# Kernel tuning notes

Measured on AMD Instinct MI355X. Metric: run time of the kernel, lower is better.

## Reference

```python
import jax, jax.numpy as jnp
import numpy as np

# Module hyper-parameters (from init_kwargs)
NDIM = 2
KSIZE = [3, 3]            # must be odd per ConvSP checks
DILATION = [0.05, 0.05]
RADIUS = 0.1
C_IN, C_OUT = 64, 64
B, N = 2, 2048


def _offsets():
    # Kernel-cell center offsets relative to the particle, row-major over dims
    # (matches the cartesian ordering of the original C extension).
    axes = [(np.arange(k) - (k - 1) / 2.0) * d for k, d in zip(KSIZE, DILATION)]
    grids = np.meshgrid(*axes, indexing='ij')
    return np.stack([g.reshape(-1) for g in grids], axis=-1).astype(np.float32)  # [ncells, D]


def setup_inputs() -> dict:
    key = jax.random.key(0)
    k1, k2, k3, k4, k5, k6 = jax.random.split(key, 6)
    pos = jax.random.uniform(k1, (B, N, NDIM), dtype=jnp.float32)          # coords in [0,1]^D
    invmass = jax.random.uniform(k2, (B, N), dtype=jnp.float32) * 0.9 + 0.1  # avoid 1/0
    locs = jnp.concatenate([pos, invmass[..., None]], axis=-1)             # [B,N,D+1]
    data = jax.random.normal(k3, (B, C_IN, N), dtype=jnp.float32)
    density = jax.random.uniform(k4, (B, N), dtype=jnp.float32) + 0.5      # strictly positive
    ncells = int(np.prod(KSIZE))
    weight = jax.random.normal(k5, (C_OUT, C_IN, ncells), dtype=jnp.float32) * 0.05
    bias = jax.random.normal(k6, (C_OUT,), dtype=jnp.float32) * 0.05
    return {"locs": locs, "data": data, "density": density, "weight": weight, "bias": bias}


def _convsp(locs, data, density, weight, bias):
    # SPH interpolation at each kernel-cell query point r_{i,k} = x_i + off_k:
    #   field[b,c,i,k] = sum_j (m_j / rho_j) * data[b,c,j] * W(|x_j - r_{i,k}|, RADIUS)
    # with m_j = 1/invmass_j, then a 1x1-style contraction with weight over (c,k).
    pos = locs[..., :NDIM]                               # [B,N,D]
    invmass = locs[..., NDIM]                            # [B,N]
    coef = 1.0 / (invmass * density)                     # m_j / rho_j, [B,N]
    dcoef = data * coef[:, None, :]                      # [B,C,N]
    diff = pos[:, :, None, :] - pos[:, None, :, :]       # x_i - x_j, [B,N,N,D]
    r2 = RADIUS * RADIUS
    knorm = 315.0 / (64.0 * np.pi * RADIUS ** 9)         # poly6 smoothing kernel norm
    offs = _offsets()                                    # [ncells, D]
    bsz, n = pos.shape[0], pos.shape[1]
    out = jnp.broadcast_to(bias[None, :, None], (bsz, weight.shape[0], n))
    for k in range(offs.shape[0]):                       # fixed small ncells=9 loop
        # |x_j - x_i - off| == |(x_i - x_j) + off|
        d2 = jnp.sum((diff + offs[k]) ** 2, axis=-1)     # [B,N,N] (i = query, j = neighbor)
        w = jnp.where(d2 < r2, (r2 - d2) ** 3, 0.0) * knorm
        field = jnp.einsum('bcj,bij->bci', dcoef, w)     # gather-weighted average
        out = out + jnp.einsum('oc,bci->boi', weight[:, :, k], field)
    return out


def reference(locs, data, density, weight, bias):
    return _convsp(locs, data, density, weight, bias)
```

## Files before the change

### kernel.cpp

```cpp
#include <hip/hip_runtime.h>
#include <hip/hip_bf16.h>
#include <stdint.h>

#define BATCH 2
#define NPTS  2048
#define CIN   64
#define COUT  64
#define NCELL 9

#define KNORM 1.5666851e9f
#define R2 0.01f

typedef __attribute__((ext_vector_type(8))) __bf16 bf16x8;
typedef __attribute__((ext_vector_type(4))) float  f32x4;

union B8 { uint4 u; bf16x8 v; };

static __device__ __forceinline__ unsigned pk2(float a, float b) {
    union { __hip_bfloat162 h; unsigned u; } cv;
    cv.h = __float22bfloat162_rn(make_float2(a, b));
    return cv.u;
}


__global__ __launch_bounds__(256) void prep_kernel(
    const float* __restrict__ locs, const float* __restrict__ data,
    const float* __restrict__ density, const float* __restrict__ weight,
    const float* __restrict__ bias,
    float2* __restrict__ posT, uint16_t* __restrict__ dC,
    uint16_t* __restrict__ WB, float* __restrict__ out)
{
    const int tid = threadIdx.x;
    const int g = blockIdx.x;
    if (g < 256) {
        int e = g * 256 + tid;
        int j4 = e & 511, bc = e >> 9;
        int b = bc >> 6;
        float4 dv = *(const float4*)(data + bc * 2048 + j4 * 4);
        float4 de = *(const float4*)(density + b * 2048 + j4 * 4);
        int jb = (b * 2048 + j4 * 4) * 3 + 2;
        float m0 = locs[jb], m1 = locs[jb + 3], m2 = locs[jb + 6], m3 = locs[jb + 9];
        float v0 = KNORM * dv.x / (m0 * de.x);
        float v1 = KNORM * dv.y / (m1 * de.y);
        float v2 = KNORM * dv.z / (m2 * de.z);
        float v3 = KNORM * dv.w / (m3 * de.w);
        *(uint2*)(dC + bc * 2048 + j4 * 4) = make_uint2(pk2(v0, v1), pk2(v2, v3));
    } else if (g < 272) {
        int jj = (g - 256) * 256 + tid;
        posT[jj] = make_float2(locs[jj * 3], locs[jj * 3 + 1]);
    } else if (g < 272 + NCELL) {
        int cell = g - 272;
        for (int it = 0; it < 16; it++) {
            int e = it * 256 + tid;
            int ks = e >> 11, ob = (e >> 9) & 3, lane = (e >> 3) & 63, jj = e & 7;
            int o = ob * 16 + (lane & 15);
            int c = ks * 32 + ((lane >> 4) & 3) * 8 + jj;
            union { __hip_bfloat16 h; uint16_t u; } cv;
            cv.h = __float2bfloat16(weight[(o * 64 + c) * 9 + cell]);
            WB[cell * 4096 + e] = cv.u;
        }
    } else {
        const int gb = g - (272 + NCELL);
#pragma unroll
        for (int r = 0; r < 2; r++) {
            int e4 = (gb * 512 + r * 256 + tid) * 4;
            float bv = bias[(e4 >> 11) & 63];
            *(float4*)(out + e4) = make_float4(bv, bv, bv, bv);
        }
    }
}

__global__ __launch_bounds__(192, 3) void conv_kernel(
    const float2* __restrict__ posT, const uint16_t* __restrict__ dC,
    const uint16_t* __restrict__ WB, float* __restrict__ out)
{
    __shared__ float sft[3][16 * 68];

    const int tid  = threadIdx.x;
    const int lane = tid & 63;
    const int wid  = tid >> 6;
    const int cl   = lane & 15;
    const int quad = lane >> 4;
    const int bx   = blockIdx.x;
    const int b    = bx >> 9;
    const int i0   = ((bx >> 2) & 127) * 16;
    const int jb0  = (bx & 3) * 512;

    const float2 pI = posT[b * 2048 + i0 + cl];
    const float pix = pI.x + (float)(wid - 1) * 0.05f;
    const float piy = pI.y;

    f32x4 acc[3][4];
#pragma unroll
    for (int m = 0; m < 3; m++)
#pragma unroll
        for (int nb = 0; nb < 4; nb++) acc[m][nb] = (f32x4){0.f, 0.f, 0.f, 0.f};

    const uint16_t* rb = dC + (b * 64 + cl) * 2048 + jb0 + quad * 8;
    const float2*  pjb = posT + b * 2048 + jb0 + quad * 8;

#pragma unroll 2
    for (int t = 0; t < 16; t++) {
        B8 bfc[4];
        bfc[0].u = *(const uint4*)(rb +  0 * 2048 + t * 32);
        bfc[1].u = *(const uint4*)(rb + 16 * 2048 + t * 32);
        bfc[2].u = *(const uint4*)(rb + 32 * 2048 + t * 32);
        bfc[3].u = *(const uint4*)(rb + 48 * 2048 + t * 32);

        const float4* pp = (const float4*)(pjb + t * 32);
        float4 q0 = pp[0], q1 = pp[1], q2 = pp[2], q3 = pp[3];

        float axv[8], dyv[8];
        axv[0] = pix - q0.x; dyv[0] = piy - q0.y;
        axv[1] = pix - q0.z; dyv[1] = piy - q0.w;
        axv[2] = pix - q1.x; dyv[2] = piy - q1.y;
        axv[3] = pix - q1.z; dyv[3] = piy - q1.w;
        axv[4] = pix - q2.x; dyv[4] = piy - q2.y;
        axv[5] = pix - q2.z; dyv[5] = piy - q2.w;
        axv[6] = pix - q3.x; dyv[6] = piy - q3.y;
        axv[7] = pix - q3.z; dyv[7] = piy - q3.w;

        float w0[8], w1[8], w2[8];
#pragma unroll
        for (int p = 0; p < 8; p++) {
            float ru = fmaf(-axv[p], axv[p], R2);
            float s  = fmaf(-dyv[p], dyv[p], ru);
            float sp = s - 0.0025f;
            float tm = fmaf( 0.1f, dyv[p], sp);
            float tp = fmaf(-0.1f, dyv[p], sp);
            float m0 = fmaxf(tm, 0.0f);
            float m1 = fmaxf(s,  0.0f);
            float m2 = fmaxf(tp, 0.0f);
            w0[p] = (m0 * m0) * m0;
            w1[p] = (m1 * m1) * m1;
            w2[p] = (m2 * m2) * m2;
        }

        B8 a0, a1, a2;
        a0.u = make_uint4(pk2(w0[0], w0[1]), pk2(w0[2], w0[3]),
                          pk2(w0[4], w0[5]), pk2(w0[6], w0[7]));
        a1.u = make_uint4(pk2(w1[0], w1[1]), pk2(w1[2], w1[3]),
                          pk2(w1[4], w1[5]), pk2(w1[6], w1[7]));
        a2.u = make_uint4(pk2(w2[0], w2[1]), pk2(w2[2], w2[3]),
                          pk2(w2[4], w2[5]), pk2(w2[6], w2[7]));

#pragma unroll
        for (int nb = 0; nb < 4; nb++) {
            acc[0][nb] = __builtin_amdgcn_mfma_f32_16x16x32_bf16(
                a0.v, bfc[nb].v, acc[0][nb], 0, 0, 0);
            acc[1][nb] = __builtin_amdgcn_mfma_f32_16x16x32_bf16(
                a1.v, bfc[nb].v, acc[1][nb], 0, 0, 0);
            acc[2][nb] = __builtin_amdgcn_mfma_f32_16x16x32_bf16(
                a2.v, bfc[nb].v, acc[2][nb], 0, 0, 0);
        }
    }

    float* scr = &sft[wid][0];
    f32x4 acc2[4];
#pragma unroll
    for (int ob = 0; ob < 4; ob++) acc2[ob] = (f32x4){0.f, 0.f, 0.f, 0.f};

#pragma unroll
    for (int m = 0; m < 3; m++) {
#pragma unroll
        for (int nb = 0; nb < 4; nb++)
#pragma unroll
            for (int r = 0; r < 4; r++)
                scr[(quad * 4 + r) * 68 + nb * 16 + cl] = acc[m][nb][r];
        int k = wid * 3 + m;
#pragma unroll
        for (int ks = 0; ks < 2; ks++) {
            const float* fp = &scr[cl * 68 + ks * 32 + quad * 8];
            float4 lo = *(const float4*)fp;
            float4 hi = *(const float4*)(fp + 4);
            B8 af;
            af.u = make_uint4(pk2(lo.x, lo.y), pk2(lo.z, lo.w),
                              pk2(hi.x, hi.y), pk2(hi.z, hi.w));
#pragma unroll
            for (int ob = 0; ob < 4; ob++) {
                B8 wf;
                wf.u = *(const uint4*)(WB + k * 4096 + (ks * 4 + ob) * 512 + lane * 8);
                acc2[ob] = __builtin_amdgcn_mfma_f32_16x16x32_bf16(
                    af.v, wf.v, acc2[ob], 0, 0, 0);
            }
        }
    }

#pragma unroll
    for (int ob = 0; ob < 4; ob++)
#pragma unroll
        for (int r = 0; r < 4; r++)
            scr[(quad * 4 + r) * 68 + ob * 16 + cl] = acc2[ob][r];
    __syncthreads();

    for (int e = tid; e < 256; e += 192) {
        int i  = e >> 4;
        int og = e & 15;
        float4 s0 = *(const float4*)&sft[0][i * 68 + og * 4];
        float4 s1 = *(const float4*)&sft[1][i * 68 + og * 4];
        float4 s2 = *(const float4*)&sft[2][i * 68 + og * 4];
        float v0 = s0.x + s1.x + s2.x;
        float v1 = s0.y + s1.y + s2.y;
        float v2 = s0.z + s1.z + s2.z;
        float v3 = s0.w + s1.w + s2.w;
        float* op = out + (b * 64 + og * 4) * 2048 + i0 + i;
        unsafeAtomicAdd(op + 0 * 2048, v0);
        unsafeAtomicAdd(op + 1 * 2048, v1);
        unsafeAtomicAdd(op + 2 * 2048, v2);
        unsafeAtomicAdd(op + 3 * 2048, v3);
    }
}

extern "C" void kernel_launch(void* const* d_in, const int* in_sizes, int n_in,
                              void* d_out, int out_size, void* d_ws, size_t ws_size,
                              hipStream_t stream)
{
    const float* locs    = (const float*)d_in[0];
    const float* data    = (const float*)d_in[1];
    const float* density = (const float*)d_in[2];
    const float* weight  = (const float*)d_in[3];
    const float* bias    = (const float*)d_in[4];
    float* out = (float*)d_out;

    float2*   posT = (float2*)d_ws;
    uint16_t* dC   = (uint16_t*)((char*)d_ws + 32768);
    uint16_t* WB   = (uint16_t*)((char*)d_ws + 32768 + 524288);

    prep_kernel<<<272 + NCELL + 128, 256, 0, stream>>>(
        locs, data, density, weight, bias, posT, dC, WB, out);
    conv_kernel<<<BATCH * 128 * 4, 192, 0, stream>>>(posT, dC, WB, out);
}
```

Baseline: 108.9 us.

## Split j-range 8 ways, stage positions in LDS, replace atomics with partial-sum reduce

The conv grid doubles by splitting the neighbour range into 8 chunks of 256 instead of 4 of 512. Each block stages its neighbour positions in shared memory and software-prefetches the next dC fragments. Float atomics into a bias-initialized output are replaced by plain partial-sum writes followed by a separate reduce kernel that adds the bias. This aims at more parallelism and occupancy (launch bounds raised to 4) and removes atomic contention, at the cost of an extra launch and extra partial-buffer traffic.

```diff
diff --git a/kernel.cpp b/kernel.cpp
--- a/kernel.cpp
+++ b/kernel.cpp
@@ -26,9 +26,8 @@
 __global__ __launch_bounds__(256) void prep_kernel(
     const float* __restrict__ locs, const float* __restrict__ data,
     const float* __restrict__ density, const float* __restrict__ weight,
-    const float* __restrict__ bias,
     float2* __restrict__ posT, uint16_t* __restrict__ dC,
-    uint16_t* __restrict__ WB, float* __restrict__ out)
+    uint16_t* __restrict__ WB)
 {
     const int tid = threadIdx.x;
     const int g = blockIdx.x;
@@ -48,7 +47,7 @@
     } else if (g < 272) {
         int jj = (g - 256) * 256 + tid;
         posT[jj] = make_float2(locs[jj * 3], locs[jj * 3 + 1]);
-    } else if (g < 272 + NCELL) {
+    } else {
         int cell = g - 272;
         for (int it = 0; it < 16; it++) {
             int e = it * 256 + tid;
@@ -59,22 +58,15 @@
             cv.h = __float2bfloat16(weight[(o * 64 + c) * 9 + cell]);
             WB[cell * 4096 + e] = cv.u;
         }
-    } else {
-        const int gb = g - (272 + NCELL);
-#pragma unroll
-        for (int r = 0; r < 2; r++) {
-            int e4 = (gb * 512 + r * 256 + tid) * 4;
-            float bv = bias[(e4 >> 11) & 63];
-            *(float4*)(out + e4) = make_float4(bv, bv, bv, bv);
-        }
-    }
-}
-
-__global__ __launch_bounds__(192, 3) void conv_kernel(
+    }
+}
+
+__global__ __launch_bounds__(192, 4) void conv_kernel(
     const float2* __restrict__ posT, const uint16_t* __restrict__ dC,
-    const uint16_t* __restrict__ WB, float* __restrict__ out)
-{
-    __shared__ float sft[3][16 * 68];
+    const uint16_t* __restrict__ WB, float* __restrict__ part)
+{
+    __shared__ float4 pjs[128];
+    __shared__ float  sft[3][16 * 68];
 
     const int tid  = threadIdx.x;
     const int lane = tid & 63;
@@ -82,9 +74,14 @@
     const int cl   = lane & 15;
     const int quad = lane >> 4;
     const int bx   = blockIdx.x;
-    const int b    = bx >> 9;
-    const int i0   = ((bx >> 2) & 127) * 16;
-    const int jb0  = (bx & 3) * 512;
+    const int b    = bx >> 10;
+    const int it   = (bx >> 3) & 127;
+    const int i0   = it * 16;
+    const int jq   = bx & 7;
+    const int jb0  = jq * 256;
+
+    if (tid < 128)
+        pjs[tid] = ((const float4*)(posT + b * 2048 + jb0))[tid];
 
     const float2 pI = posT[b * 2048 + i0 + cl];
     const float pix = pI.x + (float)(wid - 1) * 0.05f;
@@ -97,52 +94,60 @@
         for (int nb = 0; nb < 4; nb++) acc[m][nb] = (f32x4){0.f, 0.f, 0.f, 0.f};
 
     const uint16_t* rb = dC + (b * 64 + cl) * 2048 + jb0 + quad * 8;
-    const float2*  pjb = posT + b * 2048 + jb0 + quad * 8;
-
-#pragma unroll 2
-    for (int t = 0; t < 16; t++) {
-        B8 bfc[4];
-        bfc[0].u = *(const uint4*)(rb +  0 * 2048 + t * 32);
-        bfc[1].u = *(const uint4*)(rb + 16 * 2048 + t * 32);
-        bfc[2].u = *(const uint4*)(rb + 32 * 2048 + t * 32);
-        bfc[3].u = *(const uint4*)(rb + 48 * 2048 + t * 32);
-
-        const float4* pp = (const float4*)(pjb + t * 32);
+
+    B8 bfc[4];
+    bfc[0].u = *(const uint4*)(rb +  0 * 2048);
+    bfc[1].u = *(const uint4*)(rb + 16 * 2048);
+    bfc[2].u = *(const uint4*)(rb + 32 * 2048);
+    bfc[3].u = *(const uint4*)(rb + 48 * 2048);
+
+    __syncthreads();
+
+    for (int t = 0; t < 8; t++) {
+        B8 bfn[4];
+        if (t < 7) {
+            bfn[0].u = *(const uint4*)(rb +  0 * 2048 + (t + 1) * 32);
+            bfn[1].u = *(const uint4*)(rb + 16 * 2048 + (t + 1) * 32);
+            bfn[2].u = *(const uint4*)(rb + 32 * 2048 + (t + 1) * 32);
+            bfn[3].u = *(const uint4*)(rb + 48 * 2048 + (t + 1) * 32);
+        }
+
+        const float4* pp = &pjs[t * 16 + quad * 4];
         float4 q0 = pp[0], q1 = pp[1], q2 = pp[2], q3 = pp[3];
 
-        float axv[8], dyv[8];
-        axv[0] = pix - q0.x; dyv[0] = piy - q0.y;
-        axv[1] = pix - q0.z; dyv[1] = piy - q0.w;
-        axv[2] = pix - q1.x; dyv[2] = piy - q1.y;
-        axv[3] = pix - q1.z; dyv[3] = piy - q1.w;
-        axv[4] = pix - q2.x; dyv[4] = piy - q2.y;
-        axv[5] = pix - q2.z; dyv[5] = piy - q2.w;
-        axv[6] = pix - q3.x; dyv[6] = piy - q3.y;
-        axv[7] = pix - q3.z; dyv[7] = piy - q3.w;
-
-        float w0[8], w1[8], w2[8];
-#pragma unroll
-        for (int p = 0; p < 8; p++) {
-            float ru = fmaf(-axv[p], axv[p], R2);
-            float s  = fmaf(-dyv[p], dyv[p], ru);
-            float sp = s - 0.0025f;
-            float tm = fmaf( 0.1f, dyv[p], sp);
-            float tp = fmaf(-0.1f, dyv[p], sp);
-            float m0 = fmaxf(tm, 0.0f);
-            float m1 = fmaxf(s,  0.0f);
-            float m2 = fmaxf(tp, 0.0f);
-            w0[p] = (m0 * m0) * m0;
-            w1[p] = (m1 * m1) * m1;
-            w2[p] = (m2 * m2) * m2;
-        }
+        float w0a, w1a, w2a;
+        uint32_t a0u[4], a1u[4], a2u[4];
+#define GEOM(p, QX, QY)                                                        \
+        {                                                                      \
+            float ax = pix - (QX);                                             \
+            float dy = piy - (QY);                                             \
+            float ru = fmaf(-ax, ax, R2);                                      \
+            float s  = fmaf(-dy, dy, ru);                                      \
+            float sp = s - 0.0025f;                                            \
+            float tm = fmaf( 0.1f, dy, sp);                                    \
+            float tp = fmaf(-0.1f, dy, sp);                                    \
+            float m0 = fmaxf(tm, 0.0f);                                        \
+            float m1 = fmaxf(s,  0.0f);                                        \
+            float m2 = fmaxf(tp, 0.0f);                                        \
+            float v0 = (m0 * m0) * m0;                                         \
+            float v1 = (m1 * m1) * m1;                                         \
+            float v2 = (m2 * m2) * m2;                                         \
+            if ((p) & 1) {                                                     \
+                a0u[(p) >> 1] = pk2(w0a, v0);                                  \
+                a1u[(p) >> 1] = pk2(w1a, v1);                                  \
+                a2u[(p) >> 1] = pk2(w2a, v2);                                  \
+            } else { w0a = v0; w1a = v1; w2a = v2; }                           \
+        }
+        GEOM(0, q0.x, q0.y) GEOM(1, q0.z, q0.w)
+        GEOM(2, q1.x, q1.y) GEOM(3, q1.z, q1.w)
+        GEOM(4, q2.x, q2.y) GEOM(5, q2.z, q2.w)
+        GEOM(6, q3.x, q3.y) GEOM(7, q3.z, q3.w)
+#undef GEOM
 
         B8 a0, a1, a2;
-        a0.u = make_uint4(pk2(w0[0], w0[1]), pk2(w0[2], w0[3]),
-                          pk2(w0[4], w0[5]), pk2(w0[6], w0[7]));
-        a1.u = make_uint4(pk2(w1[0], w1[1]), pk2(w1[2], w1[3]),
-                          pk2(w1[4], w1[5]), pk2(w1[6], w1[7]));
-        a2.u = make_uint4(pk2(w2[0], w2[1]), pk2(w2[2], w2[3]),
-                          pk2(w2[4], w2[5]), pk2(w2[6], w2[7]));
+        a0.u = make_uint4(a0u[0], a0u[1], a0u[2], a0u[3]);
+        a1.u = make_uint4(a1u[0], a1u[1], a1u[2], a1u[3]);
+        a2.u = make_uint4(a2u[0], a2u[1], a2u[2], a2u[3]);
 
 #pragma unroll
         for (int nb = 0; nb < 4; nb++) {
@@ -153,6 +158,11 @@
             acc[2][nb] = __builtin_amdgcn_mfma_f32_16x16x32_bf16(
                 a2.v, bfc[nb].v, acc[2][nb], 0, 0, 0);
         }
+
+        if (t < 7) {
+            bfc[0] = bfn[0]; bfc[1] = bfn[1];
+            bfc[2] = bfn[2]; bfc[3] = bfn[3];
+        }
     }
 
     float* scr = &sft[wid][0];
@@ -193,22 +203,42 @@
             scr[(quad * 4 + r) * 68 + ob * 16 + cl] = acc2[ob][r];
     __syncthreads();
 
+    float* base = part + (((jq * BATCH + b) * 128 + it) << 10);
     for (int e = tid; e < 256; e += 192) {
         int i  = e >> 4;
         int og = e & 15;
         float4 s0 = *(const float4*)&sft[0][i * 68 + og * 4];
         float4 s1 = *(const float4*)&sft[1][i * 68 + og * 4];
         float4 s2 = *(const float4*)&sft[2][i * 68 + og * 4];
-        float v0 = s0.x + s1.x + s2.x;
-        float v1 = s0.y + s1.y + s2.y;
-        float v2 = s0.z + s1.z + s2.z;
-        float v3 = s0.w + s1.w + s2.w;
-        float* op = out + (b * 64 + og * 4) * 2048 + i0 + i;
-        unsafeAtomicAdd(op + 0 * 2048, v0);
-        unsafeAtomicAdd(op + 1 * 2048, v1);
-        unsafeAtomicAdd(op + 2 * 2048, v2);
-        unsafeAtomicAdd(op + 3 * 2048, v3);
-    }
+        float4 v = make_float4(s0.x + s1.x + s2.x, s0.y + s1.y + s2.y,
+                               s0.z + s1.z + s2.z, s0.w + s1.w + s2.w);
+        *(float4*)(base + i * 64 + og * 4) = v;
+    }
+}
+
+__global__ __launch_bounds__(256) void reduce_kernel(
+    const float* __restrict__ part, const float* __restrict__ bias,
+    float* __restrict__ out)
+{
+    const int e  = blockIdx.x * 256 + threadIdx.x;
+    const int i  = e & 15;
+    const int og = (e >> 4) & 15;
+    const int it = (e >> 8) & 127;
+    const int b  = e >> 15;
+
+    const float* p = part + (((b * 128 + it) << 10) + i * 64 + og * 4);
+    float4 s = *(const float4*)p;
+#pragma unroll
+    for (int jqq = 1; jqq < 8; jqq++) {
+        float4 q = *(const float4*)(p + jqq * (BATCH * 128 * 1024));
+        s.x += q.x; s.y += q.y; s.z += q.z; s.w += q.w;
+    }
+    const float4 bv = *(const float4*)(bias + og * 4);
+    float* op = out + ((b * 64 + og * 4) * 2048) + it * 16 + i;
+    op[0 * 2048] = s.x + bv.x;
+    op[1 * 2048] = s.y + bv.y;
+    op[2 * 2048] = s.z + bv.z;
+    op[3 * 2048] = s.w + bv.w;
 }
 
 extern "C" void kernel_launch(void* const* d_in, const int* in_sizes, int n_in,
@@ -225,8 +255,10 @@
     float2*   posT = (float2*)d_ws;
     uint16_t* dC   = (uint16_t*)((char*)d_ws + 32768);
     uint16_t* WB   = (uint16_t*)((char*)d_ws + 32768 + 524288);
-
-    prep_kernel<<<272 + NCELL + 128, 256, 0, stream>>>(
-        locs, data, density, weight, bias, posT, dC, WB, out);
-    conv_kernel<<<BATCH * 128 * 4, 192, 0, stream>>>(posT, dC, WB, out);
-}
+    float*    part = (float*)((char*)d_ws + 32768 + 524288 + 73728);
+
+    prep_kernel<<<272 + NCELL, 256, 0, stream>>>(
+        locs, data, density, weight, posT, dC, WB);
+    conv_kernel<<<BATCH * 128 * 8, 192, 0, stream>>>(posT, dC, WB, part);
+    reduce_kernel<<<256, 256, 0, stream>>>(part, bias, out);
+}
```

After: 101.4 us. 6.9% less time.
